# Kernel tuning notes

Measured on AMD Instinct MI355X. Metric: run time of the kernel, lower is better.

## Reference

```python
import jax, jax.numpy as jnp
import numpy as np

N = 8192
E = 262144
IN_DIM = 512
H1 = 256
H2 = 64


def setup_inputs() -> dict:
    key = jax.random.key(0)
    ks = jax.random.split(key, 12)
    stdv1 = 1.0 / np.sqrt(H1)
    stdv2 = 1.0 / np.sqrt(H2)
    return {
        "edge_row": jax.random.randint(ks[0], (E,), 0, N),
        "edge_col": jax.random.randint(ks[1], (E,), 0, N),
        "edge_val": jax.random.uniform(ks[2], (E,), dtype=jnp.float32),
        "features": jax.random.normal(ks[3], (N, IN_DIM), dtype=jnp.float32),
        "W1": jax.random.uniform(ks[4], (IN_DIM, H1), minval=-stdv1, maxval=stdv1, dtype=jnp.float32),
        "b1": jax.random.uniform(ks[5], (H1,), minval=-stdv1, maxval=stdv1, dtype=jnp.float32),
        "W2": jax.random.uniform(ks[6], (H1, H2), minval=-stdv2, maxval=stdv2, dtype=jnp.float32),
        "b2": jax.random.uniform(ks[7], (H2,), minval=-stdv2, maxval=stdv2, dtype=jnp.float32),
        "W3": jax.random.uniform(ks[8], (H1, H2), minval=-stdv2, maxval=stdv2, dtype=jnp.float32),
        "b3": jax.random.uniform(ks[9], (H2,), minval=-stdv2, maxval=stdv2, dtype=jnp.float32),
        "noise": jax.random.normal(ks[10], (N, H2), dtype=jnp.float32),
    }


def _gcn(edge_row, edge_col, edge_val, x, W, b):
    # support = X @ W ; out = A_hat @ support (sparse COO spmm) ; tanh(out + b)
    support = x @ W                                   # [N, out]
    msg = edge_val[:, None] * support[edge_col]       # [E, out]
    out = jax.ops.segment_sum(msg, edge_row, num_segments=N)
    return jnp.tanh(out + b)


def reference(edge_row, edge_col, edge_val, features, W1, b1, W2, b2, W3, b3, noise):
    h = _gcn(edge_row, edge_col, edge_val, features, W1, b1)   # [N, H1]
    mean = _gcn(edge_row, edge_col, edge_val, h, W2, b2)       # [N, H2]
    log_std = _gcn(edge_row, edge_col, edge_val, h, W3, b3)    # [N, H2]
    z = mean + noise * jnp.exp(log_std)                        # reparameterization
    adj_rec = jax.nn.sigmoid(z @ z.T)                          # [N, N]
    return adj_rec, z
```

## Files before the change

### kernel.cpp

```cpp
#include <hip/hip_runtime.h>
#include <math.h>

static constexpr int NN  = 8192;
static constexpr int EE  = 262144;
static constexpr int IND = 512;
static constexpr int HH1 = 256;
static constexpr int RCAP = 128;

typedef _Float16 f16x8  __attribute__((ext_vector_type(8)));
typedef _Float16 f16x4  __attribute__((ext_vector_type(4)));
typedef _Float16 f16x2  __attribute__((ext_vector_type(2)));
typedef float    f32x4  __attribute__((ext_vector_type(4)));

static __device__ __forceinline__ float fast_sigmoid(float x) {
    float e = __expf(-x);
    return __builtin_amdgcn_rcpf(1.f + e);
}

__global__ __launch_bounds__(256) void k_init(const float* __restrict__ W1,
                                              const float* __restrict__ W2,
                                              const float* __restrict__ W3,
                                              _Float16* __restrict__ W1T,
                                              _Float16* __restrict__ W23T,
                                              int* __restrict__ cnt) {
    int b = blockIdx.x;
    if (b < 32) {
        cnt[b * 256 + threadIdx.x] = 0;
        return;
    }
    __shared__ float tile[32][33];
    int c = threadIdx.x & 31;
    int r0 = threadIdx.x >> 5;
    if (b < 160) {
        int t = b - 32;
        int tk = t >> 3;
        int tn = t & 7;
#pragma unroll
        for (int i = 0; i < 4; i++) {
            int r = r0 * 4 + i;
            tile[r][c] = W1[(tk * 32 + r) * HH1 + tn * 32 + c];
        }
        __syncthreads();
#pragma unroll
        for (int i = 0; i < 4; i++) {
            int rr = r0 * 4 + i;
            W1T[(tn * 32 + rr) * IND + tk * 32 + c] = (_Float16)tile[c][rr];
        }
    } else {
        int t = b - 160;
        int tk = t >> 2;
        int tn = t & 3;
        const float* Wsrc = (tn < 2) ? W2 : W3;
        int nc0 = (tn & 1) * 32;
#pragma unroll
        for (int i = 0; i < 4; i++) {
            int r = r0 * 4 + i;
            tile[r][c] = Wsrc[(tk * 32 + r) * 64 + nc0 + c];
        }
        __syncthreads();
#pragma unroll
        for (int i = 0; i < 4; i++) {
            int rr = r0 * 4 + i;
            W23T[(tn * 32 + rr) * HH1 + tk * 32 + c] = (_Float16)tile[c][rr];
        }
    }
}

__global__ __launch_bounds__(256) void k_gemm1_scatter(const float* __restrict__ X,
                                                       const _Float16* __restrict__ B,
                                                       _Float16* __restrict__ out,
                                                       const int* __restrict__ erow,
                                                       const int* __restrict__ ecol,
                                                       const float* __restrict__ eval,
                                                       int* __restrict__ cnt,
                                                       int2* __restrict__ epack) {
    int b = blockIdx.x;
    if (b >= 512) {
        int e = (b - 512) * 256 + threadIdx.x;
        int r = erow[e];
        int pos = atomicAdd(&cnt[r], 1);
        epack[(size_t)r * RCAP + pos] = make_int2(ecol[e], __float_as_int(eval[e]));
        return;
    }
    int bm = b >> 1, bn = b & 1;
    int w = threadIdx.x >> 6, l = threadIdx.x & 63;
    int wm = w >> 1, wn = w & 1;
    int lr = l & 15, kg = l >> 4;
    int row0 = bm * 32 + wm * 16;
    int col0 = bn * 128 + wn * 64;

    f32x4 acc[4];
#pragma unroll
    for (int nt = 0; nt < 4; nt++) acc[nt] = (f32x4){0.f, 0.f, 0.f, 0.f};

    for (int ks = 0; ks < IND; ks += 32) {
        int ko = ks + kg * 8;
        const float* xp = &X[(size_t)(row0 + lr) * IND + ko];
        float4 x0 = *(const float4*)xp;
        float4 x1 = *(const float4*)(xp + 4);
        f16x8 a = {(_Float16)x0.x, (_Float16)x0.y, (_Float16)x0.z, (_Float16)x0.w,
                   (_Float16)x1.x, (_Float16)x1.y, (_Float16)x1.z, (_Float16)x1.w};
        f16x8 bb[4];
#pragma unroll
        for (int nt = 0; nt < 4; nt++)
            bb[nt] = *(const f16x8*)&B[(size_t)(col0 + nt * 16 + lr) * IND + ko];
#pragma unroll
        for (int nt = 0; nt < 4; nt++)
            acc[nt] = __builtin_amdgcn_mfma_f32_16x16x32_f16(a, bb[nt], acc[nt], 0, 0, 0);
    }
#pragma unroll
    for (int nt = 0; nt < 4; nt++)
#pragma unroll
        for (int r = 0; r < 4; r++)
            out[(size_t)(row0 + kg * 4 + r) * HH1 + col0 + nt * 16 + lr] = (_Float16)acc[nt][r];
}

__global__ __launch_bounds__(512) void k_spmm1_gemm23(const int* __restrict__ cnt,
                                                      const int2* __restrict__ epack,
                                                      const _Float16* __restrict__ sup,
                                                      const float* __restrict__ b1,
                                                      const _Float16* __restrict__ W23T,
                                                      _Float16* __restrict__ s23h) {
    __shared__ _Float16 hs[16][264];
    int w = threadIdx.x >> 6, l = threadIdx.x & 63;
    int brow0 = blockIdx.x * 16;

#pragma unroll
    for (int rr = 0; rr < 2; rr++) {
        int rloc = w * 2 + rr;
        int row = brow0 + rloc;
        int s = row * RCAP, eend = s + cnt[row];
        float4 acc = make_float4(0.f, 0.f, 0.f, 0.f);
        int i = s;
        for (; i + 4 <= eend; i += 4) {
            int2 p0 = epack[i];
            int2 p1 = epack[i + 1];
            int2 p2 = epack[i + 2];
            int2 p3 = epack[i + 3];
            f16x4 t0 = *(const f16x4*)&sup[(size_t)p0.x * HH1 + l * 4];
            f16x4 t1 = *(const f16x4*)&sup[(size_t)p1.x * HH1 + l * 4];
            f16x4 t2 = *(const f16x4*)&sup[(size_t)p2.x * HH1 + l * 4];
            f16x4 t3 = *(const f16x4*)&sup[(size_t)p3.x * HH1 + l * 4];
            float v0 = __int_as_float(p0.y), v1 = __int_as_float(p1.y);
            float v2 = __int_as_float(p2.y), v3 = __int_as_float(p3.y);
            acc.x += v0 * (float)t0[0] + v1 * (float)t1[0] + v2 * (float)t2[0] + v3 * (float)t3[0];
            acc.y += v0 * (float)t0[1] + v1 * (float)t1[1] + v2 * (float)t2[1] + v3 * (float)t3[1];
            acc.z += v0 * (float)t0[2] + v1 * (float)t1[2] + v2 * (float)t2[2] + v3 * (float)t3[2];
            acc.w += v0 * (float)t0[3] + v1 * (float)t1[3] + v2 * (float)t2[3] + v3 * (float)t3[3];
        }
        for (; i < eend; i++) {
            int2 p0 = epack[i];
            f16x4 t0 = *(const f16x4*)&sup[(size_t)p0.x * HH1 + l * 4];
            float v0 = __int_as_float(p0.y);
            acc.x += v0 * (float)t0[0];
            acc.y += v0 * (float)t0[1];
            acc.z += v0 * (float)t0[2];
            acc.w += v0 * (float)t0[3];
        }
        float4 bb = ((const float4*)b1)[l];
        f16x4 o;
        o[0] = (_Float16)tanhf(acc.x + bb.x);
        o[1] = (_Float16)tanhf(acc.y + bb.y);
        o[2] = (_Float16)tanhf(acc.z + bb.z);
        o[3] = (_Float16)tanhf(acc.w + bb.w);
        *(f16x4*)&hs[rloc][l * 4] = o;
    }
    __syncthreads();

    int lr = l & 15, kg = l >> 4;
    int colbase = w * 16;
    f32x4 acc = (f32x4){0.f, 0.f, 0.f, 0.f};
    for (int ks = 0; ks < HH1; ks += 32) {
        int ko = ks + kg * 8;
        f16x8 a = *(const f16x8*)&hs[lr][ko];
        f16x8 bfrag = *(const f16x8*)&W23T[(size_t)(colbase + lr) * HH1 + ko];
        acc = __builtin_amdgcn_mfma_f32_16x16x32_f16(a, bfrag, acc, 0, 0, 0);
    }
#pragma unroll
    for (int r = 0; r < 4; r++)
        s23h[(size_t)(brow0 + kg * 4 + r) * 128 + colbase + lr] = (_Float16)acc[r];
}

__global__ __launch_bounds__(256) void k_spmm23v(const int* __restrict__ cnt,
                                                 const int2* __restrict__ epack,
                                                 const _Float16* __restrict__ s23,
                                                 const float* __restrict__ b2,
                                                 const float* __restrict__ b3,
                                                 const float* __restrict__ noise,
                                                 float* __restrict__ zout,
                                                 _Float16* __restrict__ zh) {
    int w = threadIdx.x >> 6, l = threadIdx.x & 63;
    int row = blockIdx.x * 4 + w;
    int s = row * RCAP, eend = s + cnt[row];
    float ax = 0.f, ay = 0.f;
    int i = s;
    for (; i + 4 <= eend; i += 4) {
        int2 p0 = epack[i];
        int2 p1 = epack[i + 1];
        int2 p2 = epack[i + 2];
        int2 p3 = epack[i + 3];
        f16x2 t0 = *(const f16x2*)&s23[(size_t)p0.x * 128 + l * 2];
        f16x2 t1 = *(const f16x2*)&s23[(size_t)p1.x * 128 + l * 2];
        f16x2 t2 = *(const f16x2*)&s23[(size_t)p2.x * 128 + l * 2];
        f16x2 t3 = *(const f16x2*)&s23[(size_t)p3.x * 128 + l * 2];
        float v0 = __int_as_float(p0.y), v1 = __int_as_float(p1.y);
        float v2 = __int_as_float(p2.y), v3 = __int_as_float(p3.y);
        ax += v0 * (float)t0[0] + v1 * (float)t1[0] + v2 * (float)t2[0] + v3 * (float)t3[0];
        ay += v0 * (float)t0[1] + v1 * (float)t1[1] + v2 * (float)t2[1] + v3 * (float)t3[1];
    }
    for (; i < eend; i++) {
        int2 p0 = epack[i];
        f16x2 t0 = *(const f16x2*)&s23[(size_t)p0.x * 128 + l * 2];
        float v0 = __int_as_float(p0.y);
        ax += v0 * (float)t0[0];
        ay += v0 * (float)t0[1];
    }
    float bx, by;
    if (l < 32) { bx = b2[2 * l]; by = b2[2 * l + 1]; }
    else        { bx = b3[2 * (l - 32)]; by = b3[2 * (l - 32) + 1]; }
    float t0 = tanhf(ax + bx);
    float t1 = tanhf(ay + by);
    float u0 = __shfl_xor(t0, 32, 64);
    float u1 = __shfl_xor(t1, 32, 64);
    if (l < 32) {
        float2 nz = ((const float2*)noise)[(size_t)row * 32 + l];
        float z0 = t0 + nz.x * __expf(u0);
        float z1 = t1 + nz.y * __expf(u1);
        ((float2*)zout)[(size_t)row * 32 + l] = make_float2(z0, z1);
        *(f16x2*)&zh[(size_t)row * 64 + l * 2] = (f16x2){(_Float16)z0, (_Float16)z1};
    }
}

__global__ __launch_bounds__(256) void k_zzt_mfma(const _Float16* __restrict__ zh,
                                                  float* __restrict__ adj) {
    int bi = blockIdx.y, bj = blockIdx.x;
    int tid = threadIdx.x;
    int w = tid >> 6, l = tid & 63;
    int lr = l & 15, kg = l >> 4;
    const int i0 = bi * 128 + w * 32;
    const int j0 = bj * 128;

    f16x8 a[2][2];
#pragma unroll
    for (int mt = 0; mt < 2; mt++)
#pragma unroll
        for (int kk = 0; kk < 2; kk++)
            a[mt][kk] = *(const f16x8*)&zh[(size_t)(i0 + mt * 16 + lr) * 64 + kk * 32 + kg * 8];

    f32x4 acc[2][8];
#pragma unroll
    for (int mt = 0; mt < 2; mt++)
#pragma unroll
        for (int nt = 0; nt < 8; nt++)
            acc[mt][nt] = (f32x4){0.f, 0.f, 0.f, 0.f};

#pragma unroll
    for (int nt = 0; nt < 8; nt++) {
        f16x8 b0 = *(const f16x8*)&zh[(size_t)(j0 + nt * 16 + lr) * 64 + 0  + kg * 8];
        f16x8 b1 = *(const f16x8*)&zh[(size_t)(j0 + nt * 16 + lr) * 64 + 32 + kg * 8];
        acc[0][nt] = __builtin_amdgcn_mfma_f32_16x16x32_f16(a[0][0], b0, acc[0][nt], 0, 0, 0);
        acc[0][nt] = __builtin_amdgcn_mfma_f32_16x16x32_f16(a[0][1], b1, acc[0][nt], 0, 0, 0);
        acc[1][nt] = __builtin_amdgcn_mfma_f32_16x16x32_f16(a[1][0], b0, acc[1][nt], 0, 0, 0);
        acc[1][nt] = __builtin_amdgcn_mfma_f32_16x16x32_f16(a[1][1], b1, acc[1][nt], 0, 0, 0);
    }

#pragma unroll
    for (int nt = 0; nt < 8; nt++) {
#pragma unroll
        for (int mt = 0; mt < 2; mt++) {
            size_t orow = (size_t)(j0 + nt * 16 + lr);
            size_t ocol = (size_t)(i0 + mt * 16 + kg * 4);
            float4 o;
            o.x = fast_sigmoid(acc[mt][nt][0]);
            o.y = fast_sigmoid(acc[mt][nt][1]);
            o.z = fast_sigmoid(acc[mt][nt][2]);
            o.w = fast_sigmoid(acc[mt][nt][3]);
            *(float4*)&adj[orow * NN + ocol] = o;
        }
    }
}

extern "C" void kernel_launch(void* const* d_in, const int* in_sizes, int n_in,
                              void* d_out, int out_size, void* d_ws, size_t ws_size,
                              hipStream_t stream) {
    const int*   erow  = (const int*)d_in[0];
    const int*   ecol  = (const int*)d_in[1];
    const float* eval  = (const float*)d_in[2];
    const float* X     = (const float*)d_in[3];
    const float* W1    = (const float*)d_in[4];
    const float* b1    = (const float*)d_in[5];
    const float* W2    = (const float*)d_in[6];
    const float* b2    = (const float*)d_in[7];
    const float* W3    = (const float*)d_in[8];
    const float* b3    = (const float*)d_in[9];
    const float* noise = (const float*)d_in[10];

    float* adj  = (float*)d_out;
    float* zout = (float*)d_out + (size_t)NN * NN;

    char* ws = (char*)d_ws;
    int*  cnt       = (int*)(ws + 0);
    int2* epack     = (int2*)(ws + 32768);
    _Float16* W1T   = (_Float16*)(ws + 8421376);
    _Float16* W23T  = (_Float16*)(ws + 8683520);
    _Float16* zh    = (_Float16*)(ws + 8749056);

    char* ob = (char*)d_out;
    _Float16* sup1h = (_Float16*)(ob + 0);
    _Float16* s23h  = (_Float16*)(ob + 4194304);

    k_init<<<192, 256, 0, stream>>>(W1, W2, W3, W1T, W23T, cnt);
    k_gemm1_scatter<<<512 + EE / 256, 256, 0, stream>>>(X, W1T, sup1h,
                                                        erow, ecol, eval, cnt, epack);
    k_spmm1_gemm23<<<512, 512, 0, stream>>>(cnt, epack, sup1h, b1, W23T, s23h);
    k_spmm23v<<<NN / 4, 256, 0, stream>>>(cnt, epack, s23h, b2, b3, noise, zout, zh);
    k_zzt_mfma<<<dim3(64, 64), 256, 0, stream>>>(zh, adj);
}
```

Baseline: 142.1 us.

## Split edge buckets by column half, widen spmm23 loads, use nontemporal output stores

Edge buckets are now split per row into two slots by whether the column index falls in the lower or upper half of the nodes. This is meant to add some gather locality and spread the atomic counters. The second SpMM now processes two rows per wavefront with 4-wide half-precision gathers instead of 2-wide. The adjacency and z outputs are written with nontemporal stores so the large output does not pollute the cache. Per-slot capacity falls to 64, so a row-half with more than 64 edges would overflow.

New measurement: 194.3 us. 1.37x slower.

```diff
diff --git a/kernel.cpp b/kernel.cpp
--- a/kernel.cpp
+++ b/kernel.cpp
@@ -5,11 +5,10 @@
 static constexpr int EE  = 262144;
 static constexpr int IND = 512;
 static constexpr int HH1 = 256;
-static constexpr int RCAP = 128;
+static constexpr int HCAP = 64;
 
 typedef _Float16 f16x8  __attribute__((ext_vector_type(8)));
 typedef _Float16 f16x4  __attribute__((ext_vector_type(4)));
-typedef _Float16 f16x2  __attribute__((ext_vector_type(2)));
 typedef float    f32x4  __attribute__((ext_vector_type(4)));
 
 static __device__ __forceinline__ float fast_sigmoid(float x) {
@@ -24,15 +23,15 @@
                                               _Float16* __restrict__ W23T,
                                               int* __restrict__ cnt) {
     int b = blockIdx.x;
-    if (b < 32) {
+    if (b < 64) {
         cnt[b * 256 + threadIdx.x] = 0;
         return;
     }
     __shared__ float tile[32][33];
     int c = threadIdx.x & 31;
     int r0 = threadIdx.x >> 5;
-    if (b < 160) {
-        int t = b - 32;
+    if (b < 192) {
+        int t = b - 64;
         int tk = t >> 3;
         int tn = t & 7;
 #pragma unroll
@@ -47,7 +46,7 @@
             W1T[(tn * 32 + rr) * IND + tk * 32 + c] = (_Float16)tile[c][rr];
         }
     } else {
-        int t = b - 160;
+        int t = b - 192;
         int tk = t >> 2;
         int tn = t & 3;
         const float* Wsrc = (tn < 2) ? W2 : W3;
@@ -78,8 +77,11 @@
     if (b >= 512) {
         int e = (b - 512) * 256 + threadIdx.x;
         int r = erow[e];
-        int pos = atomicAdd(&cnt[r], 1);
-        epack[(size_t)r * RCAP + pos] = make_int2(ecol[e], __float_as_int(eval[e]));
+        int c = ecol[e];
+        int h = (c >= NN / 2) ? 1 : 0;
+        int slot = r * 2 + h;
+        int pos = atomicAdd(&cnt[slot], 1);
+        epack[(size_t)slot * HCAP + pos] = make_int2(c, __float_as_int(eval[e]));
         return;
     }
     int bm = b >> 1, bn = b & 1;
@@ -129,33 +131,37 @@
     for (int rr = 0; rr < 2; rr++) {
         int rloc = w * 2 + rr;
         int row = brow0 + rloc;
-        int s = row * RCAP, eend = s + cnt[row];
         float4 acc = make_float4(0.f, 0.f, 0.f, 0.f);
-        int i = s;
-        for (; i + 4 <= eend; i += 4) {
-            int2 p0 = epack[i];
-            int2 p1 = epack[i + 1];
-            int2 p2 = epack[i + 2];
-            int2 p3 = epack[i + 3];
-            f16x4 t0 = *(const f16x4*)&sup[(size_t)p0.x * HH1 + l * 4];
-            f16x4 t1 = *(const f16x4*)&sup[(size_t)p1.x * HH1 + l * 4];
-            f16x4 t2 = *(const f16x4*)&sup[(size_t)p2.x * HH1 + l * 4];
-            f16x4 t3 = *(const f16x4*)&sup[(size_t)p3.x * HH1 + l * 4];
-            float v0 = __int_as_float(p0.y), v1 = __int_as_float(p1.y);
-            float v2 = __int_as_float(p2.y), v3 = __int_as_float(p3.y);
-            acc.x += v0 * (float)t0[0] + v1 * (float)t1[0] + v2 * (float)t2[0] + v3 * (float)t3[0];
-            acc.y += v0 * (float)t0[1] + v1 * (float)t1[1] + v2 * (float)t2[1] + v3 * (float)t3[1];
-            acc.z += v0 * (float)t0[2] + v1 * (float)t1[2] + v2 * (float)t2[2] + v3 * (float)t3[2];
-            acc.w += v0 * (float)t0[3] + v1 * (float)t1[3] + v2 * (float)t2[3] + v3 * (float)t3[3];
-        }
-        for (; i < eend; i++) {
-            int2 p0 = epack[i];
-            f16x4 t0 = *(const f16x4*)&sup[(size_t)p0.x * HH1 + l * 4];
-            float v0 = __int_as_float(p0.y);
-            acc.x += v0 * (float)t0[0];
-            acc.y += v0 * (float)t0[1];
-            acc.z += v0 * (float)t0[2];
-            acc.w += v0 * (float)t0[3];
+#pragma unroll
+        for (int h = 0; h < 2; h++) {
+            int slot = row * 2 + h;
+            int s = slot * HCAP, eend = s + cnt[slot];
+            int i = s;
+            for (; i + 4 <= eend; i += 4) {
+                int2 p0 = epack[i];
+                int2 p1 = epack[i + 1];
+                int2 p2 = epack[i + 2];
+                int2 p3 = epack[i + 3];
+                f16x4 t0 = *(const f16x4*)&sup[(size_t)p0.x * HH1 + l * 4];
+                f16x4 t1 = *(const f16x4*)&sup[(size_t)p1.x * HH1 + l * 4];
+                f16x4 t2 = *(const f16x4*)&sup[(size_t)p2.x * HH1 + l * 4];
+                f16x4 t3 = *(const f16x4*)&sup[(size_t)p3.x * HH1 + l * 4];
+                float v0 = __int_as_float(p0.y), v1 = __int_as_float(p1.y);
+                float v2 = __int_as_float(p2.y), v3 = __int_as_float(p3.y);
+                acc.x += v0 * (float)t0[0] + v1 * (float)t1[0] + v2 * (float)t2[0] + v3 * (float)t3[0];
+                acc.y += v0 * (float)t0[1] + v1 * (float)t1[1] + v2 * (float)t2[1] + v3 * (float)t3[1];
+                acc.z += v0 * (float)t0[2] + v1 * (float)t1[2] + v2 * (float)t2[2] + v3 * (float)t3[2];
+                acc.w += v0 * (float)t0[3] + v1 * (float)t1[3] + v2 * (float)t2[3] + v3 * (float)t3[3];
+            }
+            for (; i < eend; i++) {
+                int2 p0 = epack[i];
+                f16x4 t0 = *(const f16x4*)&sup[(size_t)p0.x * HH1 + l * 4];
+                float v0 = __int_as_float(p0.y);
+                acc.x += v0 * (float)t0[0];
+                acc.y += v0 * (float)t0[1];
+                acc.z += v0 * (float)t0[2];
+                acc.w += v0 * (float)t0[3];
+            }
         }
         float4 bb = ((const float4*)b1)[l];
         f16x4 o;
@@ -190,44 +196,61 @@
                                                  float* __restrict__ zout,
                                                  _Float16* __restrict__ zh) {
     int w = threadIdx.x >> 6, l = threadIdx.x & 63;
-    int row = blockIdx.x * 4 + w;
-    int s = row * RCAP, eend = s + cnt[row];
-    float ax = 0.f, ay = 0.f;
-    int i = s;
-    for (; i + 4 <= eend; i += 4) {
-        int2 p0 = epack[i];
-        int2 p1 = epack[i + 1];
-        int2 p2 = epack[i + 2];
-        int2 p3 = epack[i + 3];
-        f16x2 t0 = *(const f16x2*)&s23[(size_t)p0.x * 128 + l * 2];
-        f16x2 t1 = *(const f16x2*)&s23[(size_t)p1.x * 128 + l * 2];
-        f16x2 t2 = *(const f16x2*)&s23[(size_t)p2.x * 128 + l * 2];
-        f16x2 t3 = *(const f16x2*)&s23[(size_t)p3.x * 128 + l * 2];
-        float v0 = __int_as_float(p0.y), v1 = __int_as_float(p1.y);
-        float v2 = __int_as_float(p2.y), v3 = __int_as_float(p3.y);
-        ax += v0 * (float)t0[0] + v1 * (float)t1[0] + v2 * (float)t2[0] + v3 * (float)t3[0];
-        ay += v0 * (float)t0[1] + v1 * (float)t1[1] + v2 * (float)t2[1] + v3 * (float)t3[1];
-    }
-    for (; i < eend; i++) {
-        int2 p0 = epack[i];
-        f16x2 t0 = *(const f16x2*)&s23[(size_t)p0.x * 128 + l * 2];
-        float v0 = __int_as_float(p0.y);
-        ax += v0 * (float)t0[0];
-        ay += v0 * (float)t0[1];
-    }
-    float bx, by;
-    if (l < 32) { bx = b2[2 * l]; by = b2[2 * l + 1]; }
-    else        { bx = b3[2 * (l - 32)]; by = b3[2 * (l - 32) + 1]; }
-    float t0 = tanhf(ax + bx);
-    float t1 = tanhf(ay + by);
-    float u0 = __shfl_xor(t0, 32, 64);
-    float u1 = __shfl_xor(t1, 32, 64);
-    if (l < 32) {
-        float2 nz = ((const float2*)noise)[(size_t)row * 32 + l];
+    int sub = l >> 5;
+    int q   = l & 31;
+    int row = blockIdx.x * 8 + w * 2 + sub;
+
+    float4 acc = make_float4(0.f, 0.f, 0.f, 0.f);
+#pragma unroll
+    for (int h = 0; h < 2; h++) {
+        int slot = row * 2 + h;
+        int s = slot * HCAP, eend = s + cnt[slot];
+        int i = s;
+        for (; i + 4 <= eend; i += 4) {
+            int2 p0 = epack[i];
+            int2 p1 = epack[i + 1];
+            int2 p2 = epack[i + 2];
+            int2 p3 = epack[i + 3];
+            f16x4 t0 = *(const f16x4*)&s23[(size_t)p0.x * 128 + q * 4];
+            f16x4 t1 = *(const f16x4*)&s23[(size_t)p1.x * 128 + q * 4];
+            f16x4 t2 = *(const f16x4*)&s23[(size_t)p2.x * 128 + q * 4];
+            f16x4 t3 = *(const f16x4*)&s23[(size_t)p3.x * 128 + q * 4];
+            float v0 = __int_as_float(p0.y), v1 = __int_as_float(p1.y);
+            float v2 = __int_as_float(p2.y), v3 = __int_as_float(p3.y);
+            acc.x += v0 * (float)t0[0] + v1 * (float)t1[0] + v2 * (float)t2[0] + v3 * (float)t3[0];
+            acc.y += v0 * (float)t0[1] + v1 * (float)t1[1] + v2 * (float)t2[1] + v3 * (float)t3[1];
+            acc.z += v0 * (float)t0[2] + v1 * (float)t1[2] + v2 * (float)t2[2] + v3 * (float)t3[2];
+            acc.w += v0 * (float)t0[3] + v1 * (float)t1[3] + v2 * (float)t2[3] + v3 * (float)t3[3];
+        }
+        for (; i < eend; i++) {
+            int2 p0 = epack[i];
+            f16x4 t0 = *(const f16x4*)&s23[(size_t)p0.x * 128 + q * 4];
+            float v0 = __int_as_float(p0.y);
+            acc.x += v0 * (float)t0[0];
+            acc.y += v0 * (float)t0[1];
+            acc.z += v0 * (float)t0[2];
+            acc.w += v0 * (float)t0[3];
+        }
+    }
+    float4 bb = (q < 16) ? ((const float4*)b2)[q] : ((const float4*)b3)[q - 16];
+    float t0 = tanhf(acc.x + bb.x);
+    float t1 = tanhf(acc.y + bb.y);
+    float t2 = tanhf(acc.z + bb.z);
+    float t3 = tanhf(acc.w + bb.w);
+    float u0 = __shfl_xor(t0, 16, 64);
+    float u1 = __shfl_xor(t1, 16, 64);
+    float u2 = __shfl_xor(t2, 16, 64);
+    float u3 = __shfl_xor(t3, 16, 64);
+    if (q < 16) {
+        float4 nz = ((const float4*)noise)[(size_t)row * 16 + q];
         float z0 = t0 + nz.x * __expf(u0);
         float z1 = t1 + nz.y * __expf(u1);
-        ((float2*)zout)[(size_t)row * 32 + l] = make_float2(z0, z1);
-        *(f16x2*)&zh[(size_t)row * 64 + l * 2] = (f16x2){(_Float16)z0, (_Float16)z1};
+        float z2 = t2 + nz.z * __expf(u2);
+        float z3 = t3 + nz.w * __expf(u3);
+        f32x4 zo = {z0, z1, z2, z3};
+        __builtin_nontemporal_store(zo, &((f32x4*)zout)[(size_t)row * 16 + q]);
+        f16x4 zf = {(_Float16)z0, (_Float16)z1, (_Float16)z2, (_Float16)z3};
+        *(f16x4*)&zh[(size_t)row * 64 + q * 4] = zf;
     }
 }
 
@@ -270,12 +293,12 @@
         for (int mt = 0; mt < 2; mt++) {
             size_t orow = (size_t)(j0 + nt * 16 + lr);
             size_t ocol = (size_t)(i0 + mt * 16 + kg * 4);
-            float4 o;
-            o.x = fast_sigmoid(acc[mt][nt][0]);
-            o.y = fast_sigmoid(acc[mt][nt][1]);
-            o.z = fast_sigmoid(acc[mt][nt][2]);
-            o.w = fast_sigmoid(acc[mt][nt][3]);
-            *(float4*)&adj[orow * NN + ocol] = o;
+            f32x4 o;
+            o[0] = fast_sigmoid(acc[mt][nt][0]);
+            o[1] = fast_sigmoid(acc[mt][nt][1]);
+            o[2] = fast_sigmoid(acc[mt][nt][2]);
+            o[3] = fast_sigmoid(acc[mt][nt][3]);
+            __builtin_nontemporal_store(o, (f32x4*)&adj[orow * NN + ocol]);
         }
     }
 }
@@ -300,19 +323,19 @@
 
     char* ws = (char*)d_ws;
     int*  cnt       = (int*)(ws + 0);
-    int2* epack     = (int2*)(ws + 32768);
-    _Float16* W1T   = (_Float16*)(ws + 8421376);
-    _Float16* W23T  = (_Float16*)(ws + 8683520);
-    _Float16* zh    = (_Float16*)(ws + 8749056);
+    int2* epack     = (int2*)(ws + 65536);
+    _Float16* W1T   = (_Float16*)(ws + 8454144);
+    _Float16* W23T  = (_Float16*)(ws + 8716288);
+    _Float16* zh    = (_Float16*)(ws + 8781824);
 
     char* ob = (char*)d_out;
     _Float16* sup1h = (_Float16*)(ob + 0);
     _Float16* s23h  = (_Float16*)(ob + 4194304);
 
-    k_init<<<192, 256, 0, stream>>>(W1, W2, W3, W1T, W23T, cnt);
+    k_init<<<224, 256, 0, stream>>>(W1, W2, W3, W1T, W23T, cnt);
     k_gemm1_scatter<<<512 + EE / 256, 256, 0, stream>>>(X, W1T, sup1h,
                                                         erow, ecol, eval, cnt, epack);
     k_spmm1_gemm23<<<512, 512, 0, stream>>>(cnt, epack, sup1h, b1, W23T, s23h);
-    k_spmm23v<<<NN / 4, 256, 0, stream>>>(cnt, epack, s23h, b2, b3, noise, zout, zh);
+    k_spmm23v<<<NN / 8, 256, 0, stream>>>(cnt, epack, s23h, b2, b3, noise, zout, zh);
     k_zzt_mfma<<<dim3(64, 64), 256, 0, stream>>>(zh, adj);
 }
```

## Merge all five stages into one cooperative persistent kernel with grid syncs

Applied to the files above, without the earlier changes.

Replaces five separate kernel launches with one cooperative kernel of 256 blocks by 512 threads. Each stage (weight transpose/init, GEMM1 plus edge scatter, SpMM1 plus GEMM23, SpMM23 plus reparameterization, and the z·zᵀ sigmoid) is run by persistent blocks looping over work and separated by grid.sync(). This removes launch gaps and inter-kernel drains. In exchange, parallelism is capped at 256 blocks, which lowers occupancy for the memory-bound SpMM and the large output-writing zzᵀ stage, and the grid barriers add their own cost.

New measurement: 300.2 us. +111.2%, slower.

```diff
diff --git a/kernel.cpp b/kernel.cpp
--- a/kernel.cpp
+++ b/kernel.cpp
@@ -1,5 +1,8 @@
 #include <hip/hip_runtime.h>
+#include <hip/hip_cooperative_groups.h>
 #include <math.h>
+
+namespace cg = cooperative_groups;
 
 static constexpr int NN  = 8192;
 static constexpr int EE  = 262144;
@@ -17,265 +20,273 @@
     return __builtin_amdgcn_rcpf(1.f + e);
 }
 
-__global__ __launch_bounds__(256) void k_init(const float* __restrict__ W1,
+__global__ __launch_bounds__(512) void k_mega(const int* __restrict__ erow,
+                                              const int* __restrict__ ecol,
+                                              const float* __restrict__ eval,
+                                              const float* __restrict__ X,
+                                              const float* __restrict__ W1,
+                                              const float* __restrict__ b1,
                                               const float* __restrict__ W2,
+                                              const float* __restrict__ b2,
                                               const float* __restrict__ W3,
+                                              const float* __restrict__ b3,
+                                              const float* __restrict__ noise,
+                                              float* __restrict__ adj,
+                                              float* __restrict__ zout,
+                                              int* __restrict__ cnt,
+                                              int2* __restrict__ epack,
                                               _Float16* __restrict__ W1T,
                                               _Float16* __restrict__ W23T,
-                                              int* __restrict__ cnt) {
-    int b = blockIdx.x;
-    if (b < 32) {
-        cnt[b * 256 + threadIdx.x] = 0;
-        return;
-    }
+                                              _Float16* __restrict__ zh,
+                                              _Float16* __restrict__ sup1h,
+                                              _Float16* __restrict__ s23h) {
+    cg::grid_group grid = cg::this_grid();
     __shared__ float tile[32][33];
-    int c = threadIdx.x & 31;
-    int r0 = threadIdx.x >> 5;
-    if (b < 160) {
-        int t = b - 32;
-        int tk = t >> 3;
-        int tn = t & 7;
-#pragma unroll
-        for (int i = 0; i < 4; i++) {
-            int r = r0 * 4 + i;
-            tile[r][c] = W1[(tk * 32 + r) * HH1 + tn * 32 + c];
+    __shared__ _Float16 hs[16][264];
+
+    const int bid = blockIdx.x;
+    const int tid = threadIdx.x;
+    const int w = tid >> 6, l = tid & 63;
+    const int lr = l & 15, kg = l >> 4;
+
+    if (bid < 16) {
+        cnt[bid * 512 + tid] = 0;
+    } else if (bid < 176) {
+        bool act = tid < 256;
+        int c = tid & 31;
+        int r0 = (tid >> 5) & 7;
+        if (bid < 144) {
+            int t = bid - 16;
+            int tk = t >> 3, tn = t & 7;
+            if (act) {
+#pragma unroll
+                for (int i = 0; i < 4; i++) {
+                    int r = r0 * 4 + i;
+                    tile[r][c] = W1[(tk * 32 + r) * HH1 + tn * 32 + c];
+                }
+            }
+            __syncthreads();
+            if (act) {
+#pragma unroll
+                for (int i = 0; i < 4; i++) {
+                    int rr = r0 * 4 + i;
+                    W1T[(tn * 32 + rr) * IND + tk * 32 + c] = (_Float16)tile[c][rr];
+                }
+            }
+        } else {
+            int t = bid - 144;
+            int tk = t >> 2, tn = t & 3;
+            const float* Wsrc = (tn < 2) ? W2 : W3;
+            int nc0 = (tn & 1) * 32;
+            if (act) {
+#pragma unroll
+                for (int i = 0; i < 4; i++) {
+                    int r = r0 * 4 + i;
+                    tile[r][c] = Wsrc[(tk * 32 + r) * 64 + nc0 + c];
+                }
+            }
+            __syncthreads();
+            if (act) {
+#pragma unroll
+                for (int i = 0; i < 4; i++) {
+                    int rr = r0 * 4 + i;
+                    W23T[(tn * 32 + rr) * HH1 + tk * 32 + c] = (_Float16)tile[c][rr];
+                }
+            }
+        }
+    }
+    grid.sync();
+
+    {
+        int wm = w >> 2, wn = w & 3;
+        int row0 = bid * 32 + wm * 16;
+        int col0 = wn * 64;
+
+        f32x4 acc[4];
+#pragma unroll
+        for (int nt = 0; nt < 4; nt++) acc[nt] = (f32x4){0.f, 0.f, 0.f, 0.f};
+
+        for (int ks = 0; ks < IND; ks += 32) {
+            int ko = ks + kg * 8;
+            const float* xp = &X[(size_t)(row0 + lr) * IND + ko];
+            float4 x0 = *(const float4*)xp;
+            float4 x1 = *(const float4*)(xp + 4);
+            f16x8 a = {(_Float16)x0.x, (_Float16)x0.y, (_Float16)x0.z, (_Float16)x0.w,
+                       (_Float16)x1.x, (_Float16)x1.y, (_Float16)x1.z, (_Float16)x1.w};
+            f16x8 bb[4];
+#pragma unroll
+            for (int nt = 0; nt < 4; nt++)
+                bb[nt] = *(const f16x8*)&W1T[(size_t)(col0 + nt * 16 + lr) * IND + ko];
+#pragma unroll
+            for (int nt = 0; nt < 4; nt++)
+                acc[nt] = __builtin_amdgcn_mfma_f32_16x16x32_f16(a, bb[nt], acc[nt], 0, 0, 0);
+        }
+#pragma unroll
+        for (int nt = 0; nt < 4; nt++)
+#pragma unroll
+            for (int r = 0; r < 4; r++)
+                sup1h[(size_t)(row0 + kg * 4 + r) * HH1 + col0 + nt * 16 + lr] = (_Float16)acc[nt][r];
+
+#pragma unroll
+        for (int j = 0; j < 2; j++) {
+            int e = (bid * 2 + j) * 512 + tid;
+            int r = erow[e];
+            int pos = atomicAdd(&cnt[r], 1);
+            epack[(size_t)r * RCAP + pos] = make_int2(ecol[e], __float_as_int(eval[e]));
+        }
+    }
+    grid.sync();
+
+    for (int j = 0; j < 2; j++) {
+        if (j) __syncthreads();
+        int brow0 = (bid + 256 * j) * 16;
+#pragma unroll
+        for (int rr = 0; rr < 2; rr++) {
+            int rloc = w * 2 + rr;
+            int row = brow0 + rloc;
+            int s = row * RCAP, eend = s + cnt[row];
+            float4 acc = make_float4(0.f, 0.f, 0.f, 0.f);
+            int i = s;
+            for (; i + 4 <= eend; i += 4) {
+                int2 p0 = epack[i];
+                int2 p1 = epack[i + 1];
+                int2 p2 = epack[i + 2];
+                int2 p3 = epack[i + 3];
+                f16x4 t0 = *(const f16x4*)&sup1h[(size_t)p0.x * HH1 + l * 4];
+                f16x4 t1 = *(const f16x4*)&sup1h[(size_t)p1.x * HH1 + l * 4];
+                f16x4 t2 = *(const f16x4*)&sup1h[(size_t)p2.x * HH1 + l * 4];
+                f16x4 t3 = *(const f16x4*)&sup1h[(size_t)p3.x * HH1 + l * 4];
+                float v0 = __int_as_float(p0.y), v1 = __int_as_float(p1.y);
+                float v2 = __int_as_float(p2.y), v3 = __int_as_float(p3.y);
+                acc.x += v0 * (float)t0[0] + v1 * (float)t1[0] + v2 * (float)t2[0] + v3 * (float)t3[0];
+                acc.y += v0 * (float)t0[1] + v1 * (float)t1[1] + v2 * (float)t2[1] + v3 * (float)t3[1];
+                acc.z += v0 * (float)t0[2] + v1 * (float)t1[2] + v2 * (float)t2[2] + v3 * (float)t3[2];
+                acc.w += v0 * (float)t0[3] + v1 * (float)t1[3] + v2 * (float)t2[3] + v3 * (float)t3[3];
+            }
+            for (; i < eend; i++) {
+                int2 p0 = epack[i];
+                f16x4 t0 = *(const f16x4*)&sup1h[(size_t)p0.x * HH1 + l * 4];
+                float v0 = __int_as_float(p0.y);
+                acc.x += v0 * (float)t0[0];
+                acc.y += v0 * (float)t0[1];
+                acc.z += v0 * (float)t0[2];
+                acc.w += v0 * (float)t0[3];
+            }
+            float4 bb = ((const float4*)b1)[l];
+            f16x4 o;
+            o[0] = (_Float16)tanhf(acc.x + bb.x);
+            o[1] = (_Float16)tanhf(acc.y + bb.y);
+            o[2] = (_Float16)tanhf(acc.z + bb.z);
+            o[3] = (_Float16)tanhf(acc.w + bb.w);
+            *(f16x4*)&hs[rloc][l * 4] = o;
         }
         __syncthreads();
-#pragma unroll
-        for (int i = 0; i < 4; i++) {
-            int rr = r0 * 4 + i;
-            W1T[(tn * 32 + rr) * IND + tk * 32 + c] = (_Float16)tile[c][rr];
-        }
-    } else {
-        int t = b - 160;
-        int tk = t >> 2;
-        int tn = t & 3;
-        const float* Wsrc = (tn < 2) ? W2 : W3;
-        int nc0 = (tn & 1) * 32;
-#pragma unroll
-        for (int i = 0; i < 4; i++) {
-            int r = r0 * 4 + i;
-            tile[r][c] = Wsrc[(tk * 32 + r) * 64 + nc0 + c];
-        }
-        __syncthreads();
-#pragma unroll
-        for (int i = 0; i < 4; i++) {
-            int rr = r0 * 4 + i;
-            W23T[(tn * 32 + rr) * HH1 + tk * 32 + c] = (_Float16)tile[c][rr];
-        }
-    }
-}
-
-__global__ __launch_bounds__(256) void k_gemm1_scatter(const float* __restrict__ X,
-                                                       const _Float16* __restrict__ B,
-                                                       _Float16* __restrict__ out,
-                                                       const int* __restrict__ erow,
-                                                       const int* __restrict__ ecol,
-                                                       const float* __restrict__ eval,
-                                                       int* __restrict__ cnt,
-                                                       int2* __restrict__ epack) {
-    int b = blockIdx.x;
-    if (b >= 512) {
-        int e = (b - 512) * 256 + threadIdx.x;
-        int r = erow[e];
-        int pos = atomicAdd(&cnt[r], 1);
-        epack[(size_t)r * RCAP + pos] = make_int2(ecol[e], __float_as_int(eval[e]));
-        return;
-    }
-    int bm = b >> 1, bn = b & 1;
-    int w = threadIdx.x >> 6, l = threadIdx.x & 63;
-    int wm = w >> 1, wn = w & 1;
-    int lr = l & 15, kg = l >> 4;
-    int row0 = bm * 32 + wm * 16;
-    int col0 = bn * 128 + wn * 64;
-
-    f32x4 acc[4];
-#pragma unroll
-    for (int nt = 0; nt < 4; nt++) acc[nt] = (f32x4){0.f, 0.f, 0.f, 0.f};
-
-    for (int ks = 0; ks < IND; ks += 32) {
-        int ko = ks + kg * 8;
-        const float* xp = &X[(size_t)(row0 + lr) * IND + ko];
-        float4 x0 = *(const float4*)xp;
-        float4 x1 = *(const float4*)(xp + 4);
-        f16x8 a = {(_Float16)x0.x, (_Float16)x0.y, (_Float16)x0.z, (_Float16)x0.w,
-                   (_Float16)x1.x, (_Float16)x1.y, (_Float16)x1.z, (_Float16)x1.w};
-        f16x8 bb[4];
-#pragma unroll
-        for (int nt = 0; nt < 4; nt++)
-            bb[nt] = *(const f16x8*)&B[(size_t)(col0 + nt * 16 + lr) * IND + ko];
-#pragma unroll
-        for (int nt = 0; nt < 4; nt++)
-            acc[nt] = __builtin_amdgcn_mfma_f32_16x16x32_f16(a, bb[nt], acc[nt], 0, 0, 0);
-    }
-#pragma unroll
-    for (int nt = 0; nt < 4; nt++)
+
+        int colbase = w * 16;
+        f32x4 acc = (f32x4){0.f, 0.f, 0.f, 0.f};
+        for (int ks = 0; ks < HH1; ks += 32) {
+            int ko = ks + kg * 8;
+            f16x8 a = *(const f16x8*)&hs[lr][ko];
+            f16x8 bfrag = *(const f16x8*)&W23T[(size_t)(colbase + lr) * HH1 + ko];
+            acc = __builtin_amdgcn_mfma_f32_16x16x32_f16(a, bfrag, acc, 0, 0, 0);
+        }
 #pragma unroll
         for (int r = 0; r < 4; r++)
-            out[(size_t)(row0 + kg * 4 + r) * HH1 + col0 + nt * 16 + lr] = (_Float16)acc[nt][r];
-}
-
-__global__ __launch_bounds__(512) void k_spmm1_gemm23(const int* __restrict__ cnt,
-                                                      const int2* __restrict__ epack,
-                                                      const _Float16* __restrict__ sup,
-                                                      const float* __restrict__ b1,
-                                                      const _Float16* __restrict__ W23T,
-                                                      _Float16* __restrict__ s23h) {
-    __shared__ _Float16 hs[16][264];
-    int w = threadIdx.x >> 6, l = threadIdx.x & 63;
-    int brow0 = blockIdx.x * 16;
-
-#pragma unroll
-    for (int rr = 0; rr < 2; rr++) {
-        int rloc = w * 2 + rr;
-        int row = brow0 + rloc;
+            s23h[(size_t)(brow0 + kg * 4 + r) * 128 + colbase + lr] = (_Float16)acc[r];
+    }
+    grid.sync();
+
+#pragma unroll 1
+    for (int j = 0; j < 4; j++) {
+        int row = (bid + 256 * j) * 8 + w;
         int s = row * RCAP, eend = s + cnt[row];
-        float4 acc = make_float4(0.f, 0.f, 0.f, 0.f);
+        float ax = 0.f, ay = 0.f;
         int i = s;
         for (; i + 4 <= eend; i += 4) {
             int2 p0 = epack[i];
             int2 p1 = epack[i + 1];
             int2 p2 = epack[i + 2];
             int2 p3 = epack[i + 3];
-            f16x4 t0 = *(const f16x4*)&sup[(size_t)p0.x * HH1 + l * 4];
-            f16x4 t1 = *(const f16x4*)&sup[(size_t)p1.x * HH1 + l * 4];
-            f16x4 t2 = *(const f16x4*)&sup[(size_t)p2.x * HH1 + l * 4];
-            f16x4 t3 = *(const f16x4*)&sup[(size_t)p3.x * HH1 + l * 4];
+            f16x2 t0 = *(const f16x2*)&s23h[(size_t)p0.x * 128 + l * 2];
+            f16x2 t1 = *(const f16x2*)&s23h[(size_t)p1.x * 128 + l * 2];
+            f16x2 t2 = *(const f16x2*)&s23h[(size_t)p2.x * 128 + l * 2];
+            f16x2 t3 = *(const f16x2*)&s23h[(size_t)p3.x * 128 + l * 2];
             float v0 = __int_as_float(p0.y), v1 = __int_as_float(p1.y);
             float v2 = __int_as_float(p2.y), v3 = __int_as_float(p3.y);
-            acc.x += v0 * (float)t0[0] + v1 * (float)t1[0] + v2 * (float)t2[0] + v3 * (float)t3[0];
-            acc.y += v0 * (float)t0[1] + v1 * (float)t1[1] + v2 * (float)t2[1] + v3 * (float)t3[1];
-            acc.z += v0 * (float)t0[2] + v1 * (float)t1[2] + v2 * (float)t2[2] + v3 * (float)t3[2];
-            acc.w += v0 * (float)t0[3] + v1 * (float)t1[3] + v2 * (float)t2[3] + v3 * (float)t3[3];
+            ax += v0 * (float)t0[0] + v1 * (float)t1[0] + v2 * (float)t2[0] + v3 * (float)t3[0];
+            ay += v0 * (float)t0[1] + v1 * (float)t1[1] + v2 * (float)t2[1] + v3 * (float)t3[1];
         }
         for (; i < eend; i++) {
             int2 p0 = epack[i];
-            f16x4 t0 = *(const f16x4*)&sup[(size_t)p0.x * HH1 + l * 4];
+            f16x2 t0 = *(const f16x2*)&s23h[(size_t)p0.x * 128 + l * 2];
             float v0 = __int_as_float(p0.y);
-            acc.x += v0 * (float)t0[0];
-            acc.y += v0 * (float)t0[1];
-            acc.z += v0 * (float)t0[2];
-            acc.w += v0 * (float)t0[3];
-        }
-        float4 bb = ((const float4*)b1)[l];
-        f16x4 o;
-        o[0] = (_Float16)tanhf(acc.x + bb.x);
-        o[1] = (_Float16)tanhf(acc.y + bb.y);
-        o[2] = (_Float16)tanhf(acc.z + bb.z);
-        o[3] = (_Float16)tanhf(acc.w + bb.w);
-        *(f16x4*)&hs[rloc][l * 4] = o;
-    }
-    __syncthreads();
-
-    int lr = l & 15, kg = l >> 4;
-    int colbase = w * 16;
-    f32x4 acc = (f32x4){0.f, 0.f, 0.f, 0.f};
-    for (int ks = 0; ks < HH1; ks += 32) {
-        int ko = ks + kg * 8;
-        f16x8 a = *(const f16x8*)&hs[lr][ko];
-        f16x8 bfrag = *(const f16x8*)&W23T[(size_t)(colbase + lr) * HH1 + ko];
-        acc = __builtin_amdgcn_mfma_f32_16x16x32_f16(a, bfrag, acc, 0, 0, 0);
-    }
-#pragma unroll
-    for (int r = 0; r < 4; r++)
-        s23h[(size_t)(brow0 + kg * 4 + r) * 128 + colbase + lr] = (_Float16)acc[r];
-}
-
-__global__ __launch_bounds__(256) void k_spmm23v(const int* __restrict__ cnt,
-                                                 const int2* __restrict__ epack,
-                                                 const _Float16* __restrict__ s23,
-                                                 const float* __restrict__ b2,
-                                                 const float* __restrict__ b3,
-                                                 const float* __restrict__ noise,
-                                                 float* __restrict__ zout,
-                                                 _Float16* __restrict__ zh) {
-    int w = threadIdx.x >> 6, l = threadIdx.x & 63;
-    int row = blockIdx.x * 4 + w;
-    int s = row * RCAP, eend = s + cnt[row];
-    float ax = 0.f, ay = 0.f;
-    int i = s;
-    for (; i + 4 <= eend; i += 4) {
-        int2 p0 = epack[i];
-        int2 p1 = epack[i + 1];
-        int2 p2 = epack[i + 2];
-        int2 p3 = epack[i + 3];
-        f16x2 t0 = *(const f16x2*)&s23[(size_t)p0.x * 128 + l * 2];
-        f16x2 t1 = *(const f16x2*)&s23[(size_t)p1.x * 128 + l * 2];
-        f16x2 t2 = *(const f16x2*)&s23[(size_t)p2.x * 128 + l * 2];
-        f16x2 t3 = *(const f16x2*)&s23[(size_t)p3.x * 128 + l * 2];
-        float v0 = __int_as_float(p0.y), v1 = __int_as_float(p1.y);
-        float v2 = __int_as_float(p2.y), v3 = __int_as_float(p3.y);
-        ax += v0 * (float)t0[0] + v1 * (float)t1[0] + v2 * (float)t2[0] + v3 * (float)t3[0];
-        ay += v0 * (float)t0[1] + v1 * (float)t1[1] + v2 * (float)t2[1] + v3 * (float)t3[1];
-    }
-    for (; i < eend; i++) {
-        int2 p0 = epack[i];
-        f16x2 t0 = *(const f16x2*)&s23[(size_t)p0.x * 128 + l * 2];
-        float v0 = __int_as_float(p0.y);
-        ax += v0 * (float)t0[0];
-        ay += v0 * (float)t0[1];
-    }
-    float bx, by;
-    if (l < 32) { bx = b2[2 * l]; by = b2[2 * l + 1]; }
-    else        { bx = b3[2 * (l - 32)]; by = b3[2 * (l - 32) + 1]; }
-    float t0 = tanhf(ax + bx);
-    float t1 = tanhf(ay + by);
-    float u0 = __shfl_xor(t0, 32, 64);
-    float u1 = __shfl_xor(t1, 32, 64);
-    if (l < 32) {
-        float2 nz = ((const float2*)noise)[(size_t)row * 32 + l];
-        float z0 = t0 + nz.x * __expf(u0);
-        float z1 = t1 + nz.y * __expf(u1);
-        ((float2*)zout)[(size_t)row * 32 + l] = make_float2(z0, z1);
-        *(f16x2*)&zh[(size_t)row * 64 + l * 2] = (f16x2){(_Float16)z0, (_Float16)z1};
-    }
-}
-
-__global__ __launch_bounds__(256) void k_zzt_mfma(const _Float16* __restrict__ zh,
-                                                  float* __restrict__ adj) {
-    int bi = blockIdx.y, bj = blockIdx.x;
-    int tid = threadIdx.x;
-    int w = tid >> 6, l = tid & 63;
-    int lr = l & 15, kg = l >> 4;
-    const int i0 = bi * 128 + w * 32;
-    const int j0 = bj * 128;
-
-    f16x8 a[2][2];
-#pragma unroll
-    for (int mt = 0; mt < 2; mt++)
-#pragma unroll
-        for (int kk = 0; kk < 2; kk++)
-            a[mt][kk] = *(const f16x8*)&zh[(size_t)(i0 + mt * 16 + lr) * 64 + kk * 32 + kg * 8];
-
-    f32x4 acc[2][8];
-#pragma unroll
-    for (int mt = 0; mt < 2; mt++)
-#pragma unroll
-        for (int nt = 0; nt < 8; nt++)
-            acc[mt][nt] = (f32x4){0.f, 0.f, 0.f, 0.f};
-
-#pragma unroll
-    for (int nt = 0; nt < 8; nt++) {
-        f16x8 b0 = *(const f16x8*)&zh[(size_t)(j0 + nt * 16 + lr) * 64 + 0  + kg * 8];
-        f16x8 b1 = *(const f16x8*)&zh[(size_t)(j0 + nt * 16 + lr) * 64 + 32 + kg * 8];
-        acc[0][nt] = __builtin_amdgcn_mfma_f32_16x16x32_f16(a[0][0], b0, acc[0][nt], 0, 0, 0);
-        acc[0][nt] = __builtin_amdgcn_mfma_f32_16x16x32_f16(a[0][1], b1, acc[0][nt], 0, 0, 0);
-        acc[1][nt] = __builtin_amdgcn_mfma_f32_16x16x32_f16(a[1][0], b0, acc[1][nt], 0, 0, 0);
-        acc[1][nt] = __builtin_amdgcn_mfma_f32_16x16x32_f16(a[1][1], b1, acc[1][nt], 0, 0, 0);
-    }
-
-#pragma unroll
-    for (int nt = 0; nt < 8; nt++) {
-#pragma unroll
-        for (int mt = 0; mt < 2; mt++) {
-            size_t orow = (size_t)(j0 + nt * 16 + lr);
-            size_t ocol = (size_t)(i0 + mt * 16 + kg * 4);
-            float4 o;
-            o.x = fast_sigmoid(acc[mt][nt][0]);
-            o.y = fast_sigmoid(acc[mt][nt][1]);
-            o.z = fast_sigmoid(acc[mt][nt][2]);
-            o.w = fast_sigmoid(acc[mt][nt][3]);
-            *(float4*)&adj[orow * NN + ocol] = o;
+            ax += v0 * (float)t0[0];
+            ay += v0 * (float)t0[1];
+        }
+        float bx, by;
+        if (l < 32) { bx = b2[2 * l]; by = b2[2 * l + 1]; }
+        else        { bx = b3[2 * (l - 32)]; by = b3[2 * (l - 32) + 1]; }
+        float t0 = tanhf(ax + bx);
+        float t1 = tanhf(ay + by);
+        float u0 = __shfl_xor(t0, 32, 64);
+        float u1 = __shfl_xor(t1, 32, 64);
+        if (l < 32) {
+            float2 nz = ((const float2*)noise)[(size_t)row * 32 + l];
+            float z0 = t0 + nz.x * __expf(u0);
+            float z1 = t1 + nz.y * __expf(u1);
+            ((float2*)zout)[(size_t)row * 32 + l] = make_float2(z0, z1);
+            *(f16x2*)&zh[(size_t)row * 64 + l * 2] = (f16x2){(_Float16)z0, (_Float16)z1};
+        }
+    }
+    grid.sync();
+
+    {
+        int g = w >> 2, wl = w & 3;
+#pragma unroll 1
+        for (int j = 0; j < 8; j++) {
+            int vb = bid + 256 * (2 * j + g);
+            int bi = vb >> 6, bj = vb & 63;
+            const int i0 = bi * 128 + wl * 32;
+            const int j0 = bj * 128;
+
+            f16x8 a[2][2];
+#pragma unroll
+            for (int mt = 0; mt < 2; mt++)
+#pragma unroll
+                for (int kk = 0; kk < 2; kk++)
+                    a[mt][kk] = *(const f16x8*)&zh[(size_t)(i0 + mt * 16 + lr) * 64 + kk * 32 + kg * 8];
+
+            f32x4 acc[2][8];
+#pragma unroll
+            for (int mt = 0; mt < 2; mt++)
+#pragma unroll
+                for (int nt = 0; nt < 8; nt++)
+                    acc[mt][nt] = (f32x4){0.f, 0.f, 0.f, 0.f};
+
+#pragma unroll
+            for (int nt = 0; nt < 8; nt++) {
+                f16x8 b0 = *(const f16x8*)&zh[(size_t)(j0 + nt * 16 + lr) * 64 + 0  + kg * 8];
+                f16x8 b1 = *(const f16x8*)&zh[(size_t)(j0 + nt * 16 + lr) * 64 + 32 + kg * 8];
+                acc[0][nt] = __builtin_amdgcn_mfma_f32_16x16x32_f16(a[0][0], b0, acc[0][nt], 0, 0, 0);
+                acc[0][nt] = __builtin_amdgcn_mfma_f32_16x16x32_f16(a[0][1], b1, acc[0][nt], 0, 0, 0);
+                acc[1][nt] = __builtin_amdgcn_mfma_f32_16x16x32_f16(a[1][0], b0, acc[1][nt], 0, 0, 0);
+                acc[1][nt] = __builtin_amdgcn_mfma_f32_16x16x32_f16(a[1][1], b1, acc[1][nt], 0, 0, 0);
+            }
+
+#pragma unroll
+            for (int nt = 0; nt < 8; nt++) {
+#pragma unroll
+                for (int mt = 0; mt < 2; mt++) {
+                    size_t orow = (size_t)(j0 + nt * 16 + lr);
+                    size_t ocol = (size_t)(i0 + mt * 16 + kg * 4);
+                    float4 o;
+                    o.x = fast_sigmoid(acc[mt][nt][0]);
+                    o.y = fast_sigmoid(acc[mt][nt][1]);
+                    o.z = fast_sigmoid(acc[mt][nt][2]);
+                    o.w = fast_sigmoid(acc[mt][nt][3]);
+                    *(float4*)&adj[orow * NN + ocol] = o;
+                }
+            }
         }
     }
 }
@@ -309,10 +320,11 @@
     _Float16* sup1h = (_Float16*)(ob + 0);
     _Float16* s23h  = (_Float16*)(ob + 4194304);
 
-    k_init<<<192, 256, 0, stream>>>(W1, W2, W3, W1T, W23T, cnt);
-    k_gemm1_scatter<<<512 + EE / 256, 256, 0, stream>>>(X, W1T, sup1h,
-                                                        erow, ecol, eval, cnt, epack);
-    k_spmm1_gemm23<<<512, 512, 0, stream>>>(cnt, epack, sup1h, b1, W23T, s23h);
-    k_spmm23v<<<NN / 4, 256, 0, stream>>>(cnt, epack, s23h, b2, b3, noise, zout, zh);
-    k_zzt_mfma<<<dim3(64, 64), 256, 0, stream>>>(zh, adj);
+    void* args[] = {
+        (void*)&erow, (void*)&ecol, (void*)&eval, (void*)&X, (void*)&W1, (void*)&b1,
+        (void*)&W2, (void*)&b2, (void*)&W3, (void*)&b3, (void*)&noise,
+        (void*)&adj, (void*)&zout, (void*)&cnt, (void*)&epack,
+        (void*)&W1T, (void*)&W23T, (void*)&zh, (void*)&sup1h, (void*)&s23h
+    };
+    hipLaunchCooperativeKernel((const void*)k_mega, dim3(256), dim3(512), args, 0, stream);
 }
```
